# Kernel optimization log

Measured on AMD Instinct MI355X. Metric: run time of the kernel, lower is better.

Reference implementation:

```python
import jax, jax.numpy as jnp
import numpy as np

B, S, T = 8, 2048, 128  # batch, seq_len, token_embedding_dim (== dep_transformed_dim, required by source bug)


def setup_inputs() -> dict:
    key = jax.random.key(0)
    k1, k2, k3, k4, k5, k6, k7 = jax.random.split(key, 7)
    sT = 1.0 / np.sqrt(T)
    sS = 1.0 / np.sqrt(S)
    return {
        "token_embeddings": jax.random.normal(k1, (B, S, T), jnp.float32),
        "dep_embeddings": jax.random.normal(k2, (B, S, T), jnp.float32),  # dead input (source bug), kept for fidelity
        "dep_heads": jax.random.randint(k3, (B, S), 0, S, jnp.int32),
        # composition_transform = Bilinear(T, T, T): weight [T_out, T_in1, T_in2], bias [T_out]
        "W_comp": jax.random.uniform(k4, (T, T, T), jnp.float32, -sT, sT),
        "b_comp": jax.random.uniform(k5, (T,), jnp.float32, -sT, sT),
        # reduction_transform = Linear(S, 1)
        "w_red": jax.random.uniform(k6, (1, S), jnp.float32, -sS, sS),
        "b_red": jax.random.uniform(k7, (1,), jnp.float32, -sS, sS),
    }


def reference(token_embeddings, dep_embeddings, dep_heads, W_comp, b_comp, w_red, b_red):
    # Faithful to source semantics (including the bug where dep_transform output is
    # discarded and tanh is applied to token_embeddings instead):
    #   dense[b,i,j,:] = tanh( bilinear(token[b,j], mask(i==heads[b,j]) * tanh(token[b,j])) )
    #   out[b,i,t]     = sum_j w_red[j] * dense[b,i,j,t] + b_red
    # Where mask is zero, bilinear collapses to its bias, so we never materialize
    # the [B,S,S,T] tensor: compute the 'active' value per token j and scatter-add
    # the delta vs. the bias-only baseline into row i = dep_heads[b,j].
    h = jnp.tanh(token_embeddings)                                   # [B,S,T]
    val = jnp.einsum('bsp,tpq,bsq->bst', token_embeddings, W_comp, h) + b_comp  # [B,S,T]
    act = jnp.tanh(val)                                              # active (masked-in) values
    base_val = jnp.tanh(b_comp)                                      # [T] value where mask is zero
    w = w_red[0]                                                     # [S], reduction weights over j
    base = jnp.sum(w) * base_val + b_red[0]                          # [T] bias-only row
    delta = w[None, :, None] * (act - base_val)                      # [B,S,T]
    b_idx = jnp.arange(token_embeddings.shape[0])[:, None]           # [B,1]
    out = base + jnp.zeros_like(act).at[b_idx, dep_heads].add(delta) # scatter over head rows
    return out
```

## Files before the change

### kernel.cpp

```cpp
#include <hip/hip_runtime.h>
#include <hip/hip_fp16.h>
#include <math.h>

#define S_LEN 2048
#define T_DIM 128
#define BM 64
#define TN 64
#define NBLK 512
#define TOKR 66

typedef _Float16 half8 __attribute__((ext_vector_type(8)));
typedef _Float16 half2t __attribute__((ext_vector_type(2)));
typedef float floatx16 __attribute__((ext_vector_type(16)));

__device__ __forceinline__ float tanh_fast(float x) {
  return 1.0f - __fdividef(2.0f, 1.0f + __expf(2.0f * x));
}

__global__ __launch_bounds__(256) void prep_kernel(
    const float* __restrict__ W, const float* __restrict__ w_red,
    const float* __restrict__ b_comp, const float* __restrict__ b_red,
    _Float16* __restrict__ W16f, float* __restrict__ out) {
  const int blk = blockIdx.x;
  const int tid = threadIdx.x;
  if (blk < 1024) {
    const int t = blk >> 3;
    const int qh = (blk >> 2) & 1;
    const int it = blk & 3;
    const int tc = t >> 5, tl = t & 31;
    const int e8 = it * 256 + tid;
    const int p = e8 >> 3;
    const int q = qh * 64 + (e8 & 7) * 8;
    const float* src = W + (size_t)t * 16384 + (size_t)p * 128 + q;
    const float4 v0 = *(const float4*)src;
    const float4 v1 = *(const float4*)(src + 4);
    half8 h;
    h[0] = (_Float16)v0.x; h[1] = (_Float16)v0.y;
    h[2] = (_Float16)v0.z; h[3] = (_Float16)v0.w;
    h[4] = (_Float16)v1.x; h[5] = (_Float16)v1.y;
    h[6] = (_Float16)v1.z; h[7] = (_Float16)v1.w;
    const int kc = q >> 4, lh2 = (q >> 3) & 1;
    *(half8*)(W16f + ((size_t)((p * 4 + tc) * 8 + kc)) * 512 + lh2 * 256 + tl * 8) = h;
  } else {
    __shared__ float red4[4];
    float part = 0.f;
#pragma unroll
    for (int i = 0; i < 8; ++i) part += w_red[tid * 8 + i];
#pragma unroll
    for (int off = 32; off > 0; off >>= 1) part += __shfl_down(part, off, 64);
    if ((tid & 63) == 0) red4[tid >> 6] = part;
    __syncthreads();
    const float Sw = red4[0] + red4[1] + red4[2] + red4[3];
    const float br = b_red[0];
    const size_t base = (size_t)(blk - 1024) * 1024 + (size_t)tid * 4;
    const int t0 = (int)(base & 127);
    float4 v;
    v.x = Sw * tanh_fast(b_comp[t0 + 0]) + br;
    v.y = Sw * tanh_fast(b_comp[t0 + 1]) + br;
    v.z = Sw * tanh_fast(b_comp[t0 + 2]) + br;
    v.w = Sw * tanh_fast(b_comp[t0 + 3]) + br;
    *(float4*)(out + base) = v;
  }
}

__global__ __launch_bounds__(512, 4) void main_kernel(
    const float* __restrict__ tok, const int* __restrict__ heads,
    const _Float16* __restrict__ W16f, const float* __restrict__ b_comp,
    const float* __restrict__ w_red, float* __restrict__ out) {
  __shared__ _Float16 tokT2[128 * TOKR];
  __shared__ float red[2][BM * TN];

  const int tid = threadIdx.x;
  const int lane = tid & 63;
  const int kh = tid >> 6;
  const int l31 = lane & 31;
  const int lh = lane >> 5;
  const int blk = blockIdx.x;
  const int th = (blk >> 1) & 1;
  const int mb = ((blk >> 2) << 1) | (blk & 1);
  const int pstag = ((blk * 53) + ((blk >> 8) << 6)) & 127;
  const size_t tokbase = (size_t)mb * BM * T_DIM;

#pragma unroll
  for (int it = 0; it < 4; ++it) {
    const int f = it * 512 + tid;
    const int m = f >> 5;
    const int p0 = (f & 31) * 4;
    const float4 v = *(const float4*)(tok + tokbase + (size_t)m * 128 + p0);
    const int mi = (m & 31) * 2 + (m >> 5);
    tokT2[(p0 + 0) * TOKR + mi] = (_Float16)v.x;
    tokT2[(p0 + 1) * TOKR + mi] = (_Float16)v.y;
    tokT2[(p0 + 2) * TOKR + mi] = (_Float16)v.z;
    tokT2[(p0 + 3) * TOKR + mi] = (_Float16)v.w;
  }

  half8 h16[2];
#pragma unroll
  for (int mh = 0; mh < 2; ++mh) {
    const int m = mh * 32 + l31;
    const int q0 = kh * 16 + lh * 8;
    const float4 v0 = *(const float4*)(tok + tokbase + (size_t)m * 128 + q0);
    const float4 v1 = *(const float4*)(tok + tokbase + (size_t)m * 128 + q0 + 4);
    h16[mh][0] = (_Float16)tanh_fast(v0.x);
    h16[mh][1] = (_Float16)tanh_fast(v0.y);
    h16[mh][2] = (_Float16)tanh_fast(v0.z);
    h16[mh][3] = (_Float16)tanh_fast(v0.w);
    h16[mh][4] = (_Float16)tanh_fast(v1.x);
    h16[mh][5] = (_Float16)tanh_fast(v1.y);
    h16[mh][6] = (_Float16)tanh_fast(v1.z);
    h16[mh][7] = (_Float16)tanh_fast(v1.w);
  }
  __syncthreads();

  int off[2];
#pragma unroll
  for (int tt = 0; tt < 2; ++tt)
    off[tt] = (((th * 2 + tt) * 8 + kh) << 9) + lane * 8;

  floatx16 acc[2][2];
#pragma unroll
  for (int mh = 0; mh < 2; ++mh)
#pragma unroll
    for (int tt = 0; tt < 2; ++tt)
#pragma unroll
      for (int r = 0; r < 16; ++r) acc[mh][tt][r] = 0.f;

  half8 bf0[2], bf1[2], bf2[2];
  half2t tk0, tk1, tk2;

  auto loadB = [&](half8 (&bf)[2], int p) {
    const int pp = (p + pstag) & 127;
    const _Float16* wp = W16f + (size_t)pp * 16384;
    bf[0] = *(const half8*)(wp + off[0]);
    bf[1] = *(const half8*)(wp + off[1]);
  };
  auto loadT = [&](half2t& tk, int p) {
    const int pp = (p + pstag) & 127;
    tk = *(const half2t*)(tokT2 + pp * TOKR + l31 * 2);
  };

  auto compute = [&](half8 (&bf)[2], half2t tk) {
    half8 a0 = h16[0] * tk[0];
    half8 a1 = h16[1] * tk[1];
    acc[0][0] = __builtin_amdgcn_mfma_f32_32x32x16_f16(a0, bf[0], acc[0][0], 0, 0, 0);
    acc[0][1] = __builtin_amdgcn_mfma_f32_32x32x16_f16(a0, bf[1], acc[0][1], 0, 0, 0);
    acc[1][0] = __builtin_amdgcn_mfma_f32_32x32x16_f16(a1, bf[0], acc[1][0], 0, 0, 0);
    acc[1][1] = __builtin_amdgcn_mfma_f32_32x32x16_f16(a1, bf[1], acc[1][1], 0, 0, 0);
  };

  loadB(bf0, 0);  loadT(tk0, 0);
  loadB(bf1, 1);  loadT(tk1, 1);
  for (int p = 0; p < 126; p += 3) {
    loadB(bf2, p + 2);  loadT(tk2, p + 2);
    compute(bf0, tk0);
    loadB(bf0, p + 3);  loadT(tk0, p + 3);
    compute(bf1, tk1);
    loadB(bf1, p + 4);  loadT(tk1, p + 4);
    compute(bf2, tk2);
  }
  compute(bf0, tk0);
  compute(bf1, tk1);

  __syncthreads();
  {
    float* R = &red[kh & 1][0];
    const int g = kh >> 1;
#pragma unroll
    for (int phase = 0; phase < 4; ++phase) {
      if (g == phase) {
#pragma unroll
        for (int mh = 0; mh < 2; ++mh)
#pragma unroll
          for (int tt = 0; tt < 2; ++tt) {
            const int t_loc = tt * 32 + l31;
#pragma unroll
            for (int r = 0; r < 16; ++r) {
              const int m_loc = mh * 32 + (r & 3) + 8 * (r >> 2) + 4 * lh;
              const int addr = m_loc * TN + t_loc;
              if (phase == 0) R[addr] = acc[mh][tt][r];
              else            R[addr] += acc[mh][tt][r];
            }
          }
      }
      __syncthreads();
    }
  }

  const int t_loc = tid & 63;
  const int mgrp = tid >> 6;
  const int t = th * 64 + t_loc;
  const float bc = b_comp[t];
  const float tb = tanh_fast(bc);
#pragma unroll 4
  for (int mi = 0; mi < 8; ++mi) {
    const int m_loc = mi * 8 + mgrp;
    const int gm = mb * BM + m_loc;
    const int head = heads[gm];
    const float wr = w_red[gm & 2047];
    const float v = red[0][m_loc * TN + t_loc] + red[1][m_loc * TN + t_loc] + bc;
    atomicAdd(out + ((size_t)(gm >> 11) * S_LEN + head) * T_DIM + t,
              wr * (tanh_fast(v) - tb));
  }
}

extern "C" void kernel_launch(void* const* d_in, const int* in_sizes, int n_in,
                              void* d_out, int out_size, void* d_ws, size_t ws_size,
                              hipStream_t stream) {
  const float* tok    = (const float*)d_in[0];
  const int*   heads  = (const int*)d_in[2];
  const float* W      = (const float*)d_in[3];
  const float* b_comp = (const float*)d_in[4];
  const float* w_red  = (const float*)d_in[5];
  const float* b_red  = (const float*)d_in[6];
  float* out = (float*)d_out;

  _Float16* W16f = (_Float16*)d_ws;

  prep_kernel<<<3072, 256, 0, stream>>>(W, w_red, b_comp, b_red, W16f, out);
  main_kernel<<<NBLK, 512, 0, stream>>>(tok, heads, W16f, b_comp, w_red, out);
}
```

Measured before the change: 152.4 us.

## Retile main kernel to 128 rows by 32 output columns per block

Each block now covers 128 token rows and 32 output features instead of 64x64. Each wave loads one W fragment per p step and reuses it across four MFMAs over the row groups, which halves the W traffic per MFMA. The p-stagger is also simplified to depend only on the row group. Register pressure (four accumulators) and shared memory for the transposed tokens go up, and the new stagger may cause more blocks to hit the same W slices at the same time.

```diff
diff --git a/kernel.cpp b/kernel.cpp
--- a/kernel.cpp
+++ b/kernel.cpp
@@ -4,13 +4,13 @@
 
 #define S_LEN 2048
 #define T_DIM 128
-#define BM 64
-#define TN 64
+#define BM 128
+#define TN 32
 #define NBLK 512
-#define TOKR 66
+#define TOKR 132
 
 typedef _Float16 half8 __attribute__((ext_vector_type(8)));
-typedef _Float16 half2t __attribute__((ext_vector_type(2)));
+typedef _Float16 half4t __attribute__((ext_vector_type(4)));
 typedef float floatx16 __attribute__((ext_vector_type(16)));
 
 __device__ __forceinline__ float tanh_fast(float x) {
@@ -76,27 +76,27 @@
   const int l31 = lane & 31;
   const int lh = lane >> 5;
   const int blk = blockIdx.x;
-  const int th = (blk >> 1) & 1;
-  const int mb = ((blk >> 2) << 1) | (blk & 1);
-  const int pstag = ((blk * 53) + ((blk >> 8) << 6)) & 127;
+  const int th = (blk >> 1) & 3;
+  const int mb = ((blk >> 3) << 1) | (blk & 1);
+  const int pstag = ((blk >> 3) * 2) & 127;
   const size_t tokbase = (size_t)mb * BM * T_DIM;
 
 #pragma unroll
-  for (int it = 0; it < 4; ++it) {
+  for (int it = 0; it < 8; ++it) {
     const int f = it * 512 + tid;
     const int m = f >> 5;
     const int p0 = (f & 31) * 4;
     const float4 v = *(const float4*)(tok + tokbase + (size_t)m * 128 + p0);
-    const int mi = (m & 31) * 2 + (m >> 5);
+    const int mi = (m & 31) * 4 + (m >> 5);
     tokT2[(p0 + 0) * TOKR + mi] = (_Float16)v.x;
     tokT2[(p0 + 1) * TOKR + mi] = (_Float16)v.y;
     tokT2[(p0 + 2) * TOKR + mi] = (_Float16)v.z;
     tokT2[(p0 + 3) * TOKR + mi] = (_Float16)v.w;
   }
 
-  half8 h16[2];
-#pragma unroll
-  for (int mh = 0; mh < 2; ++mh) {
+  half8 h16[4];
+#pragma unroll
+  for (int mh = 0; mh < 4; ++mh) {
     const int m = mh * 32 + l31;
     const int q0 = kh * 16 + lh * 8;
     const float4 v0 = *(const float4*)(tok + tokbase + (size_t)m * 128 + q0);
@@ -112,40 +112,32 @@
   }
   __syncthreads();
 
-  int off[2];
-#pragma unroll
-  for (int tt = 0; tt < 2; ++tt)
-    off[tt] = (((th * 2 + tt) * 8 + kh) << 9) + lane * 8;
-
-  floatx16 acc[2][2];
-#pragma unroll
-  for (int mh = 0; mh < 2; ++mh)
-#pragma unroll
-    for (int tt = 0; tt < 2; ++tt)
-#pragma unroll
-      for (int r = 0; r < 16; ++r) acc[mh][tt][r] = 0.f;
-
-  half8 bf0[2], bf1[2], bf2[2];
-  half2t tk0, tk1, tk2;
-
-  auto loadB = [&](half8 (&bf)[2], int p) {
+  const int off = ((th * 8 + kh) << 9) + lane * 8;
+
+  floatx16 acc[4];
+#pragma unroll
+  for (int mh = 0; mh < 4; ++mh)
+#pragma unroll
+    for (int r = 0; r < 16; ++r) acc[mh][r] = 0.f;
+
+  half8 bf0, bf1, bf2;
+  half4t tk0, tk1, tk2;
+
+  auto loadB = [&](half8& bf, int p) {
     const int pp = (p + pstag) & 127;
-    const _Float16* wp = W16f + (size_t)pp * 16384;
-    bf[0] = *(const half8*)(wp + off[0]);
-    bf[1] = *(const half8*)(wp + off[1]);
+    bf = *(const half8*)(W16f + (size_t)pp * 16384 + off);
   };
-  auto loadT = [&](half2t& tk, int p) {
+  auto loadT = [&](half4t& tk, int p) {
     const int pp = (p + pstag) & 127;
-    tk = *(const half2t*)(tokT2 + pp * TOKR + l31 * 2);
+    tk = *(const half4t*)(tokT2 + pp * TOKR + l31 * 4);
   };
 
-  auto compute = [&](half8 (&bf)[2], half2t tk) {
-    half8 a0 = h16[0] * tk[0];
-    half8 a1 = h16[1] * tk[1];
-    acc[0][0] = __builtin_amdgcn_mfma_f32_32x32x16_f16(a0, bf[0], acc[0][0], 0, 0, 0);
-    acc[0][1] = __builtin_amdgcn_mfma_f32_32x32x16_f16(a0, bf[1], acc[0][1], 0, 0, 0);
-    acc[1][0] = __builtin_amdgcn_mfma_f32_32x32x16_f16(a1, bf[0], acc[1][0], 0, 0, 0);
-    acc[1][1] = __builtin_amdgcn_mfma_f32_32x32x16_f16(a1, bf[1], acc[1][1], 0, 0, 0);
+  auto compute = [&](half8 bf, half4t tk) {
+#pragma unroll
+    for (int mh = 0; mh < 4; ++mh) {
+      half8 a = h16[mh] * tk[mh];
+      acc[mh] = __builtin_amdgcn_mfma_f32_32x32x16_f16(a, bf, acc[mh], 0, 0, 0);
+    }
   };
 
   loadB(bf0, 0);  loadT(tk0, 0);
@@ -169,31 +161,28 @@
     for (int phase = 0; phase < 4; ++phase) {
       if (g == phase) {
 #pragma unroll
-        for (int mh = 0; mh < 2; ++mh)
-#pragma unroll
-          for (int tt = 0; tt < 2; ++tt) {
-            const int t_loc = tt * 32 + l31;
-#pragma unroll
-            for (int r = 0; r < 16; ++r) {
-              const int m_loc = mh * 32 + (r & 3) + 8 * (r >> 2) + 4 * lh;
-              const int addr = m_loc * TN + t_loc;
-              if (phase == 0) R[addr] = acc[mh][tt][r];
-              else            R[addr] += acc[mh][tt][r];
-            }
+        for (int mh = 0; mh < 4; ++mh) {
+#pragma unroll
+          for (int r = 0; r < 16; ++r) {
+            const int m_loc = mh * 32 + (r & 3) + 8 * (r >> 2) + 4 * lh;
+            const int addr = m_loc * TN + l31;
+            if (phase == 0) R[addr] = acc[mh][r];
+            else            R[addr] += acc[mh][r];
           }
+        }
       }
       __syncthreads();
     }
   }
 
-  const int t_loc = tid & 63;
-  const int mgrp = tid >> 6;
-  const int t = th * 64 + t_loc;
+  const int t_loc = tid & 31;
+  const int mgrp = tid >> 5;
+  const int t = th * 32 + t_loc;
   const float bc = b_comp[t];
   const float tb = tanh_fast(bc);
 #pragma unroll 4
   for (int mi = 0; mi < 8; ++mi) {
-    const int m_loc = mi * 8 + mgrp;
+    const int m_loc = mi * 16 + mgrp;
     const int gm = mb * BM + m_loc;
     const int head = heads[gm];
     const float wr = w_red[gm & 2047];
```

Result: slower. 158.0 us (+3.6%).

## Double row tile to 128 per block to reuse each weight load twice

Applied to the files above, without the earlier changes.

Raises the per-block row tile from 64 to 128 tokens, halving the grid. Each loaded W fragment now feeds 8 MFMAs instead of 4, which halves global weight traffic. It also XOR-swizzles the transposed token tile in shared memory and issues the first B loads before the barrier. In exchange it doubles the accumulator registers (occupancy hint lowered to 2) and leaves fewer blocks to hide latency.

```diff
diff --git a/kernel.cpp b/kernel.cpp
--- a/kernel.cpp
+++ b/kernel.cpp
@@ -4,13 +4,13 @@
 
 #define S_LEN 2048
 #define T_DIM 128
-#define BM 64
+#define BM 128
 #define TN 64
-#define NBLK 512
-#define TOKR 66
+#define NBLK 256
+#define TOKR 132
 
 typedef _Float16 half8 __attribute__((ext_vector_type(8)));
-typedef _Float16 half2t __attribute__((ext_vector_type(2)));
+typedef _Float16 half4t __attribute__((ext_vector_type(4)));
 typedef float floatx16 __attribute__((ext_vector_type(16)));
 
 __device__ __forceinline__ float tanh_fast(float x) {
@@ -63,7 +63,7 @@
   }
 }
 
-__global__ __launch_bounds__(512, 4) void main_kernel(
+__global__ __launch_bounds__(512, 2) void main_kernel(
     const float* __restrict__ tok, const int* __restrict__ heads,
     const _Float16* __restrict__ W16f, const float* __restrict__ b_comp,
     const float* __restrict__ w_red, float* __restrict__ out) {
@@ -76,27 +76,30 @@
   const int l31 = lane & 31;
   const int lh = lane >> 5;
   const int blk = blockIdx.x;
-  const int th = (blk >> 1) & 1;
-  const int mb = ((blk >> 2) << 1) | (blk & 1);
-  const int pstag = ((blk * 53) + ((blk >> 8) << 6)) & 127;
+  const int th = blk & 1;
+  const int mb = blk >> 1;
+  const int pstag = ((blk >> 3) * 4) & 127;
   const size_t tokbase = (size_t)mb * BM * T_DIM;
 
 #pragma unroll
-  for (int it = 0; it < 4; ++it) {
+  for (int it = 0; it < 8; ++it) {
     const int f = it * 512 + tid;
     const int m = f >> 5;
     const int p0 = (f & 31) * 4;
     const float4 v = *(const float4*)(tok + tokbase + (size_t)m * 128 + p0);
-    const int mi = (m & 31) * 2 + (m >> 5);
-    tokT2[(p0 + 0) * TOKR + mi] = (_Float16)v.x;
-    tokT2[(p0 + 1) * TOKR + mi] = (_Float16)v.y;
-    tokT2[(p0 + 2) * TOKR + mi] = (_Float16)v.z;
-    tokT2[(p0 + 3) * TOKR + mi] = (_Float16)v.w;
-  }
-
-  half8 h16[2];
-#pragma unroll
-  for (int mh = 0; mh < 2; ++mh) {
+    const int mi = (m & 31) * 4 + (m >> 5);
+    const float vv[4] = {v.x, v.y, v.z, v.w};
+#pragma unroll
+    for (int jj = 0; jj < 4; ++jj) {
+      const int p = p0 + jj;
+      const int col = mi ^ (((p + (p >> 3)) & 7) << 2);
+      tokT2[p * TOKR + col] = (_Float16)vv[jj];
+    }
+  }
+
+  half8 h16[4];
+#pragma unroll
+  for (int mh = 0; mh < 4; ++mh) {
     const int m = mh * 32 + l31;
     const int q0 = kh * 16 + lh * 8;
     const float4 v0 = *(const float4*)(tok + tokbase + (size_t)m * 128 + q0);
@@ -110,23 +113,14 @@
     h16[mh][6] = (_Float16)tanh_fast(v1.z);
     h16[mh][7] = (_Float16)tanh_fast(v1.w);
   }
-  __syncthreads();
 
   int off[2];
 #pragma unroll
   for (int tt = 0; tt < 2; ++tt)
     off[tt] = (((th * 2 + tt) * 8 + kh) << 9) + lane * 8;
 
-  floatx16 acc[2][2];
-#pragma unroll
-  for (int mh = 0; mh < 2; ++mh)
-#pragma unroll
-    for (int tt = 0; tt < 2; ++tt)
-#pragma unroll
-      for (int r = 0; r < 16; ++r) acc[mh][tt][r] = 0.f;
-
   half8 bf0[2], bf1[2], bf2[2];
-  half2t tk0, tk1, tk2;
+  half4t tk0, tk1, tk2;
 
   auto loadB = [&](half8 (&bf)[2], int p) {
     const int pp = (p + pstag) & 127;
@@ -134,22 +128,36 @@
     bf[0] = *(const half8*)(wp + off[0]);
     bf[1] = *(const half8*)(wp + off[1]);
   };
-  auto loadT = [&](half2t& tk, int p) {
+  auto loadT = [&](half4t& tk, int p) {
     const int pp = (p + pstag) & 127;
-    tk = *(const half2t*)(tokT2 + pp * TOKR + l31 * 2);
+    const int col = (l31 * 4) ^ (((pp + (pp >> 3)) & 7) << 2);
+    tk = *(const half4t*)(tokT2 + pp * TOKR + col);
   };
 
-  auto compute = [&](half8 (&bf)[2], half2t tk) {
-    half8 a0 = h16[0] * tk[0];
-    half8 a1 = h16[1] * tk[1];
-    acc[0][0] = __builtin_amdgcn_mfma_f32_32x32x16_f16(a0, bf[0], acc[0][0], 0, 0, 0);
-    acc[0][1] = __builtin_amdgcn_mfma_f32_32x32x16_f16(a0, bf[1], acc[0][1], 0, 0, 0);
-    acc[1][0] = __builtin_amdgcn_mfma_f32_32x32x16_f16(a1, bf[0], acc[1][0], 0, 0, 0);
-    acc[1][1] = __builtin_amdgcn_mfma_f32_32x32x16_f16(a1, bf[1], acc[1][1], 0, 0, 0);
+  loadB(bf0, 0);
+  loadB(bf1, 1);
+
+  floatx16 acc[4][2];
+#pragma unroll
+  for (int mh = 0; mh < 4; ++mh)
+#pragma unroll
+    for (int tt = 0; tt < 2; ++tt)
+#pragma unroll
+      for (int r = 0; r < 16; ++r) acc[mh][tt][r] = 0.f;
+
+  __syncthreads();
+
+  auto compute = [&](half8 (&bf)[2], half4t tk) {
+#pragma unroll
+    for (int mh = 0; mh < 4; ++mh) {
+      half8 a = h16[mh] * tk[mh];
+      acc[mh][0] = __builtin_amdgcn_mfma_f32_32x32x16_f16(a, bf[0], acc[mh][0], 0, 0, 0);
+      acc[mh][1] = __builtin_amdgcn_mfma_f32_32x32x16_f16(a, bf[1], acc[mh][1], 0, 0, 0);
+    }
   };
 
-  loadB(bf0, 0);  loadT(tk0, 0);
-  loadB(bf1, 1);  loadT(tk1, 1);
+  loadT(tk0, 0);
+  loadT(tk1, 1);
   for (int p = 0; p < 126; p += 3) {
     loadB(bf2, p + 2);  loadT(tk2, p + 2);
     compute(bf0, tk0);
@@ -169,7 +177,7 @@
     for (int phase = 0; phase < 4; ++phase) {
       if (g == phase) {
 #pragma unroll
-        for (int mh = 0; mh < 2; ++mh)
+        for (int mh = 0; mh < 4; ++mh)
 #pragma unroll
           for (int tt = 0; tt < 2; ++tt) {
             const int t_loc = tt * 32 + l31;
@@ -192,7 +200,7 @@
   const float bc = b_comp[t];
   const float tb = tanh_fast(bc);
 #pragma unroll 4
-  for (int mi = 0; mi < 8; ++mi) {
+  for (int mi = 0; mi < 16; ++mi) {
     const int m_loc = mi * 8 + mgrp;
     const int gm = mb * BM + m_loc;
     const int head = heads[gm];
```

Result: no change. 151.6 us (-0.5%).
